# Kernel tuning notes

Measured on AMD Instinct MI355X. Metric: run time of the kernel, lower is better.

The kernel has to match this reference:

```python
import jax, jax.numpy as jnp
import numpy as np

# EntNet entity-memory update (Henaff et al. 2017), per selected entity i:
#   g_i      = sigmoid(s . h_i + s . w_i)                       (gate)
#   h~_i     = relu(h_i @ U^T + w_i @ V^T + s @ W^T)            (candidate)
#   h_i      = l2_normalize(h_i + g_i * h~_i)
# The original TF code loops over `indices` in Python; since each index touches a
# distinct entity slot, the updates are independent and we vectorize with a single
# gather over the entity axis and a scatter (.at[].set) back.

def setup_inputs() -> dict:
    key = jax.random.key(0)
    ks = jax.random.split(key, 6)
    B, N, D, K = 32, 1024, 1024, 512
    return {
        "encoded_sents": jax.random.normal(ks[0], (B, D), jnp.float32),
        "hiddens": jax.random.normal(ks[1], (B, N, D), jnp.float32),
        "keys": jax.random.normal(ks[2], (B, N, D), jnp.float32),
        "U": jax.random.normal(ks[3], (D, D), jnp.float32),
        "V": jax.random.normal(ks[4], (D, D), jnp.float32),
        "W": jax.random.normal(ks[5], (D, D), jnp.float32),
        "indices": jnp.arange(K, dtype=jnp.int64),
    }

def reference(encoded_sents, hiddens, keys, U, V, W, indices):
    EPS = 1e-12
    h = hiddens[:, indices, :]                     # [B,K,D] gather selected entities
    w = keys[:, indices, :]                        # [B,K,D]
    s = encoded_sents                              # [B,D]
    # gate: sigmoid(s.h_i + s.w_i) -> [B,K]
    g = jax.nn.sigmoid(jnp.einsum('bd,bkd->bk', s, h + w))
    # candidate: relu(h U^T + w V^T + s W^T) -> [B,K,D]
    h_tilde = jax.nn.relu(
        jnp.einsum('bkd,ed->bke', h, U)
        + jnp.einsum('bkd,ed->bke', w, V)
        + (s @ W.T)[:, None, :]
    )
    h_new = h + g[..., None] * h_tilde
    # tf.math.l2_normalize: x * rsqrt(max(sum(x^2), eps))
    h_new = h_new * jax.lax.rsqrt(jnp.maximum(jnp.sum(h_new * h_new, axis=-1, keepdims=True), EPS))
    # scatter updated entities back
    return hiddens.at[:, indices, :].set(h_new)
```

## Files before the change

### kernel.cpp

```cpp
#include <hip/hip_runtime.h>

constexpr int Bb = 32;
constexpr int Nn = 1024;
constexpr int Dd = 1024;
constexpr int Kk = 512;
constexpr int Mm = Bb * Kk;
constexpr int KD = 2 * Dd;
constexpr int NT = KD / 64;

using bf16x8 = __bf16 __attribute__((ext_vector_type(8)));
using f32x4  = float __attribute__((ext_vector_type(4)));

constexpr size_t WS_ABF  = 0;
constexpr size_t WS_BBF  = (size_t)Mm * KD * 2;
constexpr size_t WS_G    = WS_BBF + (size_t)Nn * KD * 2;
constexpr size_t WS_SW   = WS_G + Mm * sizeof(float);
constexpr size_t WS_RN   = WS_SW + Bb * Nn * sizeof(float);
constexpr size_t WS_MASK = WS_RN + Mm * sizeof(float);
constexpr size_t WS_CNT  = WS_MASK + Nn * sizeof(int);

__global__ __launch_bounds__(256)
void setup_kernel(const float* __restrict__ U, const float* __restrict__ V,
                  const float* __restrict__ W, const float* __restrict__ s,
                  const int* __restrict__ idx,
                  __bf16* __restrict__ Bbf, float* __restrict__ sW,
                  int* __restrict__ mask, float* __restrict__ rownorm,
                  int* __restrict__ cnt) {
  int blk = blockIdx.x, tid = threadIdx.x;
  if (blk < 1024) {
    int t = blk * 256 + tid;
    int e = t >> 8;
    int c = (t & 255) << 3;
    const float* src = (c < Dd) ? (U + (size_t)e * Dd + c)
                                : (V + (size_t)e * Dd + (c - Dd));
    f32x4 f0 = *(const f32x4*)src;
    f32x4 f1 = *(const f32x4*)(src + 4);
    bf16x8 v;
    v[0]=(__bf16)f0[0]; v[1]=(__bf16)f0[1]; v[2]=(__bf16)f0[2]; v[3]=(__bf16)f0[3];
    v[4]=(__bf16)f1[0]; v[5]=(__bf16)f1[1]; v[6]=(__bf16)f1[2]; v[7]=(__bf16)f1[3];
    *(bf16x8*)(Bbf + (size_t)e * KD + c) = v;
  } else if (blk < 1280) {
    int e = (blk - 1024) * 4 + (tid >> 6);
    int lane = tid & 63;
    const float* wp = W + (size_t)e * Dd;
    float wr[16];
#pragma unroll
    for (int c = 0; c < 4; c++) {
      f32x4 wv = *(const f32x4*)(wp + c * 256 + lane * 4);
      wr[c*4+0]=wv[0]; wr[c*4+1]=wv[1]; wr[c*4+2]=wv[2]; wr[c*4+3]=wv[3];
    }
    for (int b = 0; b < Bb; b++) {
      const float* sp = s + (size_t)b * Dd;
      float acc = 0.f;
#pragma unroll
      for (int c = 0; c < 4; c++) {
        f32x4 sv = *(const f32x4*)(sp + c * 256 + lane * 4);
        acc += sv[0]*wr[c*4+0] + sv[1]*wr[c*4+1] + sv[2]*wr[c*4+2] + sv[3]*wr[c*4+3];
      }
#pragma unroll
      for (int off = 32; off; off >>= 1) acc += __shfl_xor(acc, off);
      if (lane == 0) sW[b * Nn + e] = acc;
    }
  } else if (blk == 1280) {
#pragma unroll
    for (int q = 0; q < 4; q++) mask[tid * 4 + q] = 0;
    __syncthreads();
    mask[idx[tid]] = tid + 1;
    mask[idx[tid + 256]] = tid + 257;
  } else {
    int base = (blk - 1281) * 1024 + tid * 4;
    *(f32x4*)(rownorm + base) = f32x4{0.f, 0.f, 0.f, 0.f};
    if (blk == 1281 && tid < 64) cnt[tid] = 0;
  }
}

__global__ __launch_bounds__(256)
void prep_rows_kernel(const float* __restrict__ s,
                      const float* __restrict__ hiddens,
                      const float* __restrict__ keys,
                      const int* __restrict__ mask,
                      __bf16* __restrict__ Abf,
                      float* __restrict__ g_out,
                      float* __restrict__ out) {
  __shared__ float red[4];
  int bid = blockIdx.x;
  int b = bid >> 10, n = bid & 1023;
  int tid = threadIdx.x;
  int mk = mask[n];
  const float* hp = hiddens + (size_t)bid * Dd;
  if (mk == 0) {
    ((f32x4*)(out + (size_t)bid * Dd))[tid] = ((const f32x4*)hp)[tid];
    return;
  }
  int m = b * Kk + (mk - 1);
  const float* src = (tid < 128) ? hp : (keys + (size_t)bid * Dd);
  int d = (tid & 127) * 8;
  const float* sp = s + (size_t)b * Dd + d;
  f32x4 x0 = *(const f32x4*)(src + d);
  f32x4 x1 = *(const f32x4*)(src + d + 4);
  f32x4 s0 = *(const f32x4*)sp;
  f32x4 s1 = *(const f32x4*)(sp + 4);
  float part = s0[0]*x0[0]+s0[1]*x0[1]+s0[2]*x0[2]+s0[3]*x0[3]
             + s1[0]*x1[0]+s1[1]*x1[1]+s1[2]*x1[2]+s1[3]*x1[3];
  bf16x8 v;
  v[0]=(__bf16)x0[0]; v[1]=(__bf16)x0[1]; v[2]=(__bf16)x0[2]; v[3]=(__bf16)x0[3];
  v[4]=(__bf16)x1[0]; v[5]=(__bf16)x1[1]; v[6]=(__bf16)x1[2]; v[7]=(__bf16)x1[3];
  *(bf16x8*)(Abf + (size_t)m * KD + (tid < 128 ? 0 : Dd) + d) = v;
#pragma unroll
  for (int off = 32; off; off >>= 1) part += __shfl_xor(part, off);
  if ((tid & 63) == 0) red[tid >> 6] = part;
  __syncthreads();
  if (tid == 0) {
    float acc = red[0] + red[1] + red[2] + red[3];
    g_out[m] = 1.f / (1.f + expf(-acc));
  }
}

#define VMW(N) asm volatile("s_waitcnt vmcnt(" #N ")" ::: "memory")
#define BAR()  __builtin_amdgcn_s_barrier()
#define PRI1() __builtin_amdgcn_s_setprio(1)
#define PRI0() __builtin_amdgcn_s_setprio(0)

#define STAGE_HALF(SRC, LDSOFF, BUF, HALF, KT)                                  \
  { _Pragma("unroll")                                                           \
    for (int i_ = 0; i_ < 2; ++i_) {                                            \
      __builtin_amdgcn_global_load_lds(                                         \
        (const __attribute__((address_space(1))) void*)                         \
            ((SRC) + (size_t)((HALF)*128 + i_*64)*4096 + (size_t)(KT)*128),     \
        (__attribute__((address_space(3))) void*)                               \
            (ldsc + (LDSOFF) + (BUF)*32768 + (HALF)*16384 + i_*8192 + t16),     \
        16, 0, 0);                                                              \
    } }

#define LDA4(D, BUF, RBASE)                                                     \
  { _Pragma("unroll")                                                           \
    for (int i_ = 0; i_ < 4; ++i_) {                                            \
      const char* p_ = ldsc + (BUF)*32768 + ((RBASE) + i_*16 + lr)*128;         \
      D[i_][0] = *(const bf16x8*)(p_ + kb0);                                    \
      D[i_][1] = *(const bf16x8*)(p_ + kb1);                                    \
    } }

#define LDB2(D, BUF, RBASE)                                                     \
  { _Pragma("unroll")                                                           \
    for (int j_ = 0; j_ < 2; ++j_) {                                            \
      const char* p_ = ldsc + 65536 + (BUF)*32768 + ((RBASE) + j_*16 + lr)*128; \
      D[j_][0] = *(const bf16x8*)(p_ + kb0);                                    \
      D[j_][1] = *(const bf16x8*)(p_ + kb1);                                    \
    } }

#define MF16(IOFF, JOFF, AF, BF)                                                \
  { _Pragma("unroll")                                                           \
    for (int i_ = 0; i_ < 4; ++i_)                                              \
      { _Pragma("unroll")                                                       \
        for (int j_ = 0; j_ < 2; ++j_)                                          \
          { _Pragma("unroll")                                                   \
            for (int k_ = 0; k_ < 2; ++k_)                                      \
              acc[(IOFF)+i_][(JOFF)+j_] =                                       \
                __builtin_amdgcn_mfma_f32_16x16x32_bf16(                        \
                  AF[i_][k_], BF[j_][k_], acc[(IOFF)+i_][(JOFF)+j_], 0, 0, 0);  \
          } } }

__global__ __launch_bounds__(512, 2)
void gemm_kernel(const __bf16* __restrict__ Abf,
                 const __bf16* __restrict__ Bbf,
                 const int* __restrict__ idx,
                 const float* __restrict__ sW,
                 const float* __restrict__ g,
                 const float* __restrict__ hiddens,
                 float* __restrict__ rownorm,
                 int* __restrict__ cnt,
                 float* __restrict__ out) {
  __shared__ __bf16 lds[65536];
  char* ldsc = (char*)lds;

  const int bid = blockIdx.x;
  const int mt = bid & 63, nt = bid >> 6;
  const int m0 = mt * 256, e0 = nt * 256;
  const int tid = threadIdx.x;
  const int lane = tid & 63, wid = tid >> 6;
  const int wr = wid >> 2, wc = wid & 3;
  const int lr = lane & 15, lg = lane >> 4;

  const int t16  = tid * 16;
  const int colb = t16 & 127;
  const int r_lo = t16 >> 7;
  const int scol = colb ^ ((r_lo & 7) << 4);
  const char* Asrc = (const char*)Abf + (size_t)(m0 + r_lo) * 4096 + scol;
  const char* Bsrc = (const char*)Bbf + (size_t)(e0 + r_lo) * 4096 + scol;

  const int key = (lr & 7) << 4;
  const int kb0 = (lg * 16) ^ key;
  const int kb1 = (64 + lg * 16) ^ key;

  f32x4 acc[8][4] = {};
  bf16x8 aLo[4][2], aHi[4][2], bLo[2][2], bHi[2][2];

  STAGE_HALF(Asrc, 0,     0, 0, 0);
  STAGE_HALF(Bsrc, 65536, 0, 0, 0);
  STAGE_HALF(Asrc, 0,     0, 1, 0);
  STAGE_HALF(Bsrc, 65536, 0, 1, 0);
  VMW(4);
  BAR();

  for (int n = 0; n < NT - 1; ++n) {
    const int buf = n & 1, sbuf = buf ^ 1;
    LDA4(aLo, buf, wr * 64);
    LDB2(bLo, buf, wc * 32);
    STAGE_HALF(Asrc, 0,     sbuf, 0, n + 1);
    STAGE_HALF(Bsrc, 65536, sbuf, 0, n + 1);
    STAGE_HALF(Asrc, 0,     sbuf, 1, n + 1);
    STAGE_HALF(Bsrc, 65536, sbuf, 1, n + 1);
    VMW(10); BAR(); PRI1(); MF16(0, 0, aLo, bLo); PRI0(); BAR();
    LDA4(aHi, buf, wr * 64 + 128);
    VMW(8); BAR(); PRI1(); MF16(4, 0, aHi, bLo); PRI0(); BAR();
    LDB2(bHi, buf, wc * 32 + 128);
    BAR(); PRI1(); MF16(0, 2, aLo, bHi); PRI0(); BAR();
    VMW(4); BAR(); PRI1(); MF16(4, 2, aHi, bHi); PRI0(); BAR();
  }
  {
    const int buf = (NT - 1) & 1;
    LDA4(aLo, buf, wr * 64);
    LDB2(bLo, buf, wc * 32);
    VMW(2); BAR(); PRI1(); MF16(0, 0, aLo, bLo); PRI0(); BAR();
    LDA4(aHi, buf, wr * 64 + 128);
    VMW(0); BAR(); PRI1(); MF16(4, 0, aHi, bLo); PRI0(); BAR();
    LDB2(bHi, buf, wc * 32 + 128);
    BAR(); PRI1(); MF16(0, 2, aLo, bHi); PRI0(); BAR();
    PRI1(); MF16(4, 2, aHi, bHi); PRI0();
  }

#pragma unroll
  for (int i = 0; i < 8; ++i) {
    const int mrow = m0 + (i & 3) * 16 + wr * 64 + (i >> 2) * 128;
#pragma unroll
    for (int r = 0; r < 4; ++r) {
      int m = mrow + lg * 4 + r;
      int b = m >> 9;
      int rowidx = idx[m & (Kk - 1)];
      size_t base = ((size_t)(b * Nn + rowidx)) * Dd;
      float gg = g[m];
      float part = 0.f;
#pragma unroll
      for (int j = 0; j < 4; ++j) {
        int e = e0 + (j & 1) * 16 + wc * 32 + (j >> 1) * 128 + lr;
        float ht = acc[i][j][r] + sW[b * Nn + e];
        ht = fmaxf(ht, 0.f);
        float v = hiddens[base + e] + gg * ht;
        acc[i][j][r] = v;
        part += v * v;
      }
      part += __shfl_xor(part, 1);
      part += __shfl_xor(part, 2);
      part += __shfl_xor(part, 4);
      part += __shfl_xor(part, 8);
      if (lr == 0) atomicAdd(&rownorm[m], part);
    }
  }

  __syncthreads();
  if (tid == 0) {
    __threadfence();
    atomicAdd(&cnt[mt], 1);
    while (atomicAdd(&cnt[mt], 0) < 4) { }
  }
  __syncthreads();
  __threadfence();

#pragma unroll
  for (int i = 0; i < 8; ++i) {
    const int mrow = m0 + (i & 3) * 16 + wr * 64 + (i >> 2) * 128;
#pragma unroll
    for (int r = 0; r < 4; ++r) {
      int m = mrow + lg * 4 + r;
      int b = m >> 9;
      int rowidx = idx[m & (Kk - 1)];
      size_t base = ((size_t)(b * Nn + rowidx)) * Dd;
      float nr = 0.f;
      if (lr == 0) nr = atomicAdd(&rownorm[m], 0.0f);
      nr = __shfl(nr, lg * 16);
      nr = fmaxf(nr, 1e-12f);
      float y = rsqrtf(nr);
      y = y * (1.5f - 0.5f * nr * y * y);
#pragma unroll
      for (int j = 0; j < 4; ++j) {
        int e = e0 + (j & 1) * 16 + wc * 32 + (j >> 1) * 128 + lr;
        out[base + e] = acc[i][j][r] * y;
      }
    }
  }
}

extern "C" void kernel_launch(void* const* d_in, const int* in_sizes, int n_in,
                              void* d_out, int out_size, void* d_ws, size_t ws_size,
                              hipStream_t stream) {
  const float* s       = (const float*)d_in[0];
  const float* hiddens = (const float*)d_in[1];
  const float* keys    = (const float*)d_in[2];
  const float* U       = (const float*)d_in[3];
  const float* V       = (const float*)d_in[4];
  const float* W       = (const float*)d_in[5];
  const int*   idx     = (const int*)d_in[6];
  float* out = (float*)d_out;

  char* ws = (char*)d_ws;
  __bf16* Abf   = (__bf16*)(ws + WS_ABF);
  __bf16* Bbf   = (__bf16*)(ws + WS_BBF);
  float*  g     = (float*)(ws + WS_G);
  float*  sW    = (float*)(ws + WS_SW);
  float*  rnorm = (float*)(ws + WS_RN);
  int*    mask  = (int*)(ws + WS_MASK);
  int*    cnt   = (int*)(ws + WS_CNT);

  setup_kernel<<<1297, 256, 0, stream>>>(U, V, W, s, idx, Bbf, sW, mask, rnorm, cnt);
  prep_rows_kernel<<<Bb * Nn, 256, 0, stream>>>(s, hiddens, keys, mask, Abf, g, out);
  gemm_kernel<<<(Mm / 256) * (Nn / 256), 512, 0, stream>>>(
      Abf, Bbf, idx, sW, g, hiddens, rnorm, cnt, out);
}
```

Measured before the change: 503.0 us.

## Replace inter-block spin barrier with separate row normalization kernel

Removes the atomic counter spin-wait that made GEMM blocks sharing a row tile wait for each other's partial row norms. The GEMM epilogue now stores the unnormalized update directly, and a new kernel applies the rsqrt scaling per selected row afterwards. This removes the cross-block stall and any reliance on co-residency, but adds an extra read and write pass over the updated rows plus another launch.

```diff
diff --git a/kernel.cpp b/kernel.cpp
--- a/kernel.cpp
+++ b/kernel.cpp
@@ -17,15 +17,13 @@
 constexpr size_t WS_SW   = WS_G + Mm * sizeof(float);
 constexpr size_t WS_RN   = WS_SW + Bb * Nn * sizeof(float);
 constexpr size_t WS_MASK = WS_RN + Mm * sizeof(float);
-constexpr size_t WS_CNT  = WS_MASK + Nn * sizeof(int);
 
 __global__ __launch_bounds__(256)
 void setup_kernel(const float* __restrict__ U, const float* __restrict__ V,
                   const float* __restrict__ W, const float* __restrict__ s,
                   const int* __restrict__ idx,
                   __bf16* __restrict__ Bbf, float* __restrict__ sW,
-                  int* __restrict__ mask, float* __restrict__ rownorm,
-                  int* __restrict__ cnt) {
+                  int* __restrict__ mask, float* __restrict__ rownorm) {
   int blk = blockIdx.x, tid = threadIdx.x;
   if (blk < 1024) {
     int t = blk * 256 + tid;
@@ -70,7 +68,6 @@
   } else {
     int base = (blk - 1281) * 1024 + tid * 4;
     *(f32x4*)(rownorm + base) = f32x4{0.f, 0.f, 0.f, 0.f};
-    if (blk == 1281 && tid < 64) cnt[tid] = 0;
   }
 }
 
@@ -168,7 +165,6 @@
                  const float* __restrict__ g,
                  const float* __restrict__ hiddens,
                  float* __restrict__ rownorm,
-                 int* __restrict__ cnt,
                  float* __restrict__ out) {
   __shared__ __bf16 lds[65536];
   char* ldsc = (char*)lds;
@@ -246,7 +242,7 @@
         float ht = acc[i][j][r] + sW[b * Nn + e];
         ht = fmaxf(ht, 0.f);
         float v = hiddens[base + e] + gg * ht;
-        acc[i][j][r] = v;
+        out[base + e] = v;
         part += v * v;
       }
       part += __shfl_xor(part, 1);
@@ -256,38 +252,21 @@
       if (lr == 0) atomicAdd(&rownorm[m], part);
     }
   }
-
-  __syncthreads();
-  if (tid == 0) {
-    __threadfence();
-    atomicAdd(&cnt[mt], 1);
-    while (atomicAdd(&cnt[mt], 0) < 4) { }
-  }
-  __syncthreads();
-  __threadfence();
-
-#pragma unroll
-  for (int i = 0; i < 8; ++i) {
-    const int mrow = m0 + (i & 3) * 16 + wr * 64 + (i >> 2) * 128;
-#pragma unroll
-    for (int r = 0; r < 4; ++r) {
-      int m = mrow + lg * 4 + r;
-      int b = m >> 9;
-      int rowidx = idx[m & (Kk - 1)];
-      size_t base = ((size_t)(b * Nn + rowidx)) * Dd;
-      float nr = 0.f;
-      if (lr == 0) nr = atomicAdd(&rownorm[m], 0.0f);
-      nr = __shfl(nr, lg * 16);
-      nr = fmaxf(nr, 1e-12f);
-      float y = rsqrtf(nr);
-      y = y * (1.5f - 0.5f * nr * y * y);
-#pragma unroll
-      for (int j = 0; j < 4; ++j) {
-        int e = e0 + (j & 1) * 16 + wc * 32 + (j >> 1) * 128 + lr;
-        out[base + e] = acc[i][j][r] * y;
-      }
-    }
-  }
+}
+
+__global__ void norm_kernel(const int* __restrict__ idx,
+                            const float* __restrict__ rownorm,
+                            float* __restrict__ out) {
+  int m = blockIdx.x;
+  int b = m >> 9;
+  int rowidx = idx[m & (Kk - 1)];
+  float nr = fmaxf(rownorm[m], 1e-12f);
+  float y = rsqrtf(nr);
+  y = y * (1.5f - 0.5f * nr * y * y);
+  f32x4* p = (f32x4*)(out + ((size_t)(b * Nn + rowidx)) * Dd);
+  f32x4 v = p[threadIdx.x];
+  v[0] *= y; v[1] *= y; v[2] *= y; v[3] *= y;
+  p[threadIdx.x] = v;
 }
 
 extern "C" void kernel_launch(void* const* d_in, const int* in_sizes, int n_in,
@@ -309,10 +288,10 @@
   float*  sW    = (float*)(ws + WS_SW);
   float*  rnorm = (float*)(ws + WS_RN);
   int*    mask  = (int*)(ws + WS_MASK);
-  int*    cnt   = (int*)(ws + WS_CNT);
-
-  setup_kernel<<<1297, 256, 0, stream>>>(U, V, W, s, idx, Bbf, sW, mask, rnorm, cnt);
+
+  setup_kernel<<<1297, 256, 0, stream>>>(U, V, W, s, idx, Bbf, sW, mask, rnorm);
   prep_rows_kernel<<<Bb * Nn, 256, 0, stream>>>(s, hiddens, keys, mask, Abf, g, out);
   gemm_kernel<<<(Mm / 256) * (Nn / 256), 512, 0, stream>>>(
-      Abf, Bbf, idx, sW, g, hiddens, rnorm, cnt, out);
-}
+      Abf, Bbf, idx, sW, g, hiddens, rnorm, out);
+  norm_kernel<<<Mm, 256, 0, stream>>>(idx, rnorm, out);
+}
```

Result: faster. 483.3 us (-3.9%).
